# Kernel tuning notes

Measured on AMD Instinct MI355X. Metric: run time of the kernel, lower is better.

## Reference

```python
import jax, jax.numpy as jnp
from jax import lax
import numpy as np
jax.config.update("jax_enable_x64", True)

NUM_CLASSES = 4
RADIUS = 3
POOL = 2
HALF_D = RADIUS ** 3  # 27
_CLIP_MIN = 1e-06
_POS_ALPHA = 0.0005


def setup_inputs() -> dict:
    key = jax.random.key(0)
    k1, k2 = jax.random.split(key)
    logits = jax.random.normal(k1, (2, NUM_CLASSES, 96, 96, 96), dtype=jnp.float32)
    labels = jax.random.randint(k2, (2, 96, 96, 96), 0, NUM_CLASSES).astype(jnp.int64)
    return {"logits": logits, "labels": labels}


def _max_pool3d(x):
    # kernel=stride=POOL over the last three dims of [N,C,H,W,Z]
    return lax.reduce_window(x, -jnp.inf, lax.max,
                             (1, 1, POOL, POOL, POOL), (1, 1, POOL, POOL, POOL), 'VALID')


def _get_pair_vectors(x):
    # x: [N,C,H,W,Z] -> [N,C,HALF_D, (H-R+1)*(W-R+1)*(Z-R+1)] of shifted overlapping copies
    n, c, h, w, z = x.shape
    nh, nw, nz = h - (RADIUS - 1), w - (RADIUS - 1), z - (RADIUS - 1)
    shifts = [x[:, :, i:i + nh, j:j + nw, k:k + nz]
              for i in range(RADIUS) for j in range(RADIUS) for k in range(RADIUS)]
    return jnp.stack(shifts, axis=2).reshape(n, c, HALF_D, -1)


def reference(logits, labels):
    mask = (labels < NUM_CLASSES)                     # [N,H,W,Z] bool
    maskf = mask.astype(jnp.float32)
    onehot = jax.nn.one_hot(labels * mask, NUM_CLASSES, dtype=jnp.float32)  # [N,H,W,Z,C]
    onehot = onehot * maskf[..., None]
    onehot = jnp.transpose(onehot, (0, 4, 1, 2, 3))   # [N,C,H,W,Z]
    probs = jax.nn.sigmoid(logits) * maskf[:, None] + _CLIP_MIN

    la = _max_pool3d(onehot)
    pr = _max_pool3d(probs)

    la_v = _get_pair_vectors(la).astype(jnp.float64)  # [N,C,D,M]
    pr_v = _get_pair_vectors(pr).astype(jnp.float64)

    eye = jnp.eye(HALF_D, dtype=jnp.float64)
    la_v = la_v - la_v.mean(axis=3, keepdims=True)
    pr_v = pr_v - pr_v.mean(axis=3, keepdims=True)
    la_cov = jnp.einsum('ncdm,ncem->ncde', la_v, la_v)
    pr_cov = jnp.einsum('ncdm,ncem->ncde', pr_v, pr_v)
    pr_cov_inv = jnp.linalg.inv(pr_cov + eye * _POS_ALPHA)
    la_pr_cov = jnp.einsum('ncdm,ncem->ncde', la_v, pr_v)
    appro_var = la_cov - la_pr_cov @ pr_cov_inv @ jnp.swapaxes(la_pr_cov, -2, -1)

    chol = jnp.linalg.cholesky(appro_var + eye * _POS_ALPHA)
    diag = jnp.diagonal(chol, axis1=-2, axis2=-1)
    rmi_now = 0.5 * 2.0 * jnp.sum(jnp.log(diag + 1e-08), axis=-1)  # [N,C]
    rmi_per_class = rmi_now.reshape(-1, NUM_CLASSES).mean(axis=0).astype(jnp.float32)
    rmi_per_class = rmi_per_class / float(HALF_D)
    return jnp.sum(rmi_per_class)
```

## Files before the change

kernel.cpp:

```cpp
#include <hip/hip_runtime.h>
#include <math.h>

#define NVAL  97336
#define NCH   8
#define NREP  8
#define GSZ   20480

typedef unsigned short u16;
typedef unsigned int u32;
typedef __attribute__((ext_vector_type(8))) short bf16x8;
typedef __attribute__((ext_vector_type(4))) float f32x4;
typedef __attribute__((ext_vector_type(4))) unsigned int u32x4;

#define LINE_B 336
#define COPY_B 112
#define VOL_B  21504
#define GLINE_U16 48

__global__ __launch_bounds__(256) void pool_kernel(
    const float* __restrict__ logits, const int* __restrict__ labels,
    u16* __restrict__ shifted, float* __restrict__ gacc,
    float* __restrict__ out) {
  int t = blockIdx.x * 256 + threadIdx.x;
  if (t == 0) out[0] = 0.0f;
  for (int z = t; z < NREP * GSZ; z += 432 * 256) gacc[z] = 0.0f;
  int Zp = t % 24; int tmp = t / 24;
  int Y = tmp % 48; tmp /= 48;
  int X = tmp % 48; int n = tmp / 48;
  int sb = (2 * X) * 9216 + (2 * Y) * 96 + 4 * Zp;
  const int4* lb4 = (const int4*)(labels + n * 884736 + sb);
  int4 La = lb4[0], Lb = lb4[24], Lc = lb4[2304], Ld = lb4[2328];
  #pragma unroll
  for (int c = 0; c < 4; c++) {
    const float4* lg4 = (const float4*)(logits + (size_t)(n * 4 + c) * 884736 + sb);
    float4 v0 = lg4[0], v1 = lg4[24], v2 = lg4[2304], v3 = lg4[2328];
    float mx0 = fmaxf(fmaxf(fmaxf(v0.x, v0.y), fmaxf(v1.x, v1.y)),
                      fmaxf(fmaxf(v2.x, v2.y), fmaxf(v3.x, v3.y)));
    float mx1 = fmaxf(fmaxf(fmaxf(v0.z, v0.w), fmaxf(v1.z, v1.w)),
                      fmaxf(fmaxf(v2.z, v2.w), fmaxf(v3.z, v3.w)));
    float pr0 = 1.0f / (1.0f + expf(-mx0)) + 1e-6f;
    float pr1 = 1.0f / (1.0f + expf(-mx1)) + 1e-6f;
    int la0 = (La.x == c || La.y == c || Lb.x == c || Lb.y == c ||
               Lc.x == c || Lc.y == c || Ld.x == c || Ld.y == c);
    int la1 = (La.z == c || La.w == c || Lb.z == c || Lb.w == c ||
               Lc.z == c || Lc.w == c || Ld.z == c || Ld.w == c);
    u32 lapack = (la0 ? 0x3F80u : 0u) | (la1 ? 0x3F800000u : 0u);
    unsigned int q0 = __float_as_uint(pr0);
    unsigned int q1 = __float_as_uint(pr1);
    u32 p0 = (q0 + 0x7FFF + ((q0 >> 16) & 1)) >> 16;
    u32 p1 = (q1 + 0x7FFF + ((q1 >> 16) & 1)) & 0xFFFF0000u;
    u32 prpack = p0 | p1;
    int ch = n * 4 + c;
    int line = X * 48 + Y;
    ((u32*)shifted)[((size_t)(ch * 2 + 0) * 2304 + line) * 24 + Zp] = lapack;
    ((u32*)shifted)[((size_t)(ch * 2 + 1) * 2304 + line) * 24 + Zp] = prpack;
  }
}

#define MFMA16(A, B, C) __builtin_amdgcn_mfma_f32_16x16x32_bf16((A), (B), (C), 0, 0, 0)

#define STEP(BA, AM) do {                                                  \
    int _ba = (BA);                                                        \
    u32x4 ub0 = *(const u32x4*)(smem + _ba + laneC0);                      \
    u32x4 ub1 = *(const u32x4*)(smem + _ba + laneC1);                      \
    u32x4 ub2 = *(const u32x4*)(smem + _ba + laneC2);                      \
    u32x4 ub3 = *(const u32x4*)(smem + _ba + laneC3);                      \
    ub3 = iszero ? zer4 : (isones ? one4 : ub3);                           \
    u32x4 ua0 = ub0, ua1 = ub1, ua2 = ub2, ua3 = ub3;                      \
    ua0.w &= (AM); ua1.w &= (AM); ua2.w &= (AM); ua3.w &= (AM);            \
    bf16x8 A0 = __builtin_bit_cast(bf16x8, ua0);                           \
    bf16x8 A1 = __builtin_bit_cast(bf16x8, ua1);                           \
    bf16x8 A2 = __builtin_bit_cast(bf16x8, ua2);                           \
    bf16x8 A3 = __builtin_bit_cast(bf16x8, ua3);                           \
    bf16x8 B0 = __builtin_bit_cast(bf16x8, ub0);                           \
    bf16x8 B1 = __builtin_bit_cast(bf16x8, ub1);                           \
    bf16x8 B2 = __builtin_bit_cast(bf16x8, ub2);                           \
    bf16x8 B3 = __builtin_bit_cast(bf16x8, ub3);                           \
    acc0 = MFMA16(A0, B0, acc0);  acc1 = MFMA16(A0, B1, acc1);             \
    acc2 = MFMA16(A0, B2, acc2);  acc3 = MFMA16(A0, B3, acc3);             \
    acc4 = MFMA16(A1, B1, acc4);  acc5 = MFMA16(A1, B2, acc5);             \
    acc6 = MFMA16(A1, B3, acc6);  acc7 = MFMA16(A2, B2, acc7);             \
    acc8 = MFMA16(A2, B3, acc8);  acc9 = MFMA16(A3, B3, acc9);             \
  } while (0)

__global__ __launch_bounds__(256) void gram_kernel(
    const u16* __restrict__ shifted, float* __restrict__ gacc) {
  __shared__ __align__(16) unsigned char smem[43008];
  int bx = blockIdx.x;
  int half = bx & 1;
  int tile = (bx >> 1) & 63;
  int ch = bx >> 7;
  int xt = tile >> 3, yt = tile & 7;
  int X0 = xt * 6, Y0 = yt * 6;
  int tw = (xt == 7) ? 4 : 6, th = (yt == 7) ? 4 : 6;
  int tid = threadIdx.x;

  const u16* base = shifted + (size_t)ch * 2 * 2304 * GLINE_U16;
  for (int j = tid; j < 768; j += 256) {
    int chunk = j % 6; int li = j / 6;
    int sy = li & 7, sx = (li >> 3) & 7, vol = li >> 6;
    int gx = X0 + sx; if (gx > 47) gx = 47;
    int gy = Y0 + sy; if (gy > 47) gy = 47;
    const u32* src = (const u32*)(base +
        ((size_t)vol * 2304 + gx * 48 + gy) * GLINE_U16);
    u32x4 v = *(const u32x4*)(src + chunk * 4);
    u32 d4 = (chunk < 5) ? src[chunk * 4 + 4] : 0u;
    unsigned char* dstp = smem + vol * VOL_B + ((sx << 3) + sy) * LINE_B + chunk * 16;
    *(u32x4*)(dstp) = v;
    u32x4 s1 = { (v.x >> 16) | (v.y << 16), (v.y >> 16) | (v.z << 16),
                 (v.z >> 16) | (v.w << 16), (v.w >> 16) | (d4 << 16) };
    *(u32x4*)(dstp + COPY_B) = s1;
    u32x4 s2 = { v.y, v.z, v.w, d4 };
    *(u32x4*)(dstp + 2 * COPY_B) = s2;
  }
  __syncthreads();

  int lane = tid & 63, w = tid >> 6;
  int q = lane >> 4, rlo = lane & 15;
#define LANEC(F) ({ int _r = (F) * 16 + rlo; int _vol = 0, _s = 0;           \
    if (_r < 27) { _s = _r; } else if (_r < 54) { _vol = 1; _s = _r - 27; }  \
    int _dx = _s / 9, _dy = (_s / 3) % 3, _dz = _s % 3;                      \
    _vol * VOL_B + ((_dx << 3) + _dy) * LINE_B + _dz * COPY_B; })
  int laneC0 = LANEC(0), laneC1 = LANEC(1), laneC2 = LANEC(2), laneC3 = LANEC(3);
  unsigned int am1 = (q == 1) ? 0u : ~0u;
  unsigned int am2 = (q == 3) ? 0u : ~0u;
  bool isones = (rlo == 6);
  bool iszero = (rlo > 6);
  u32x4 one4 = {0x3F803F80u, 0x3F803F80u, 0x3F803F80u, 0x3F803F80u};
  u32x4 zer4 = {0u, 0u, 0u, 0u};

  f32x4 acc0 = {0,0,0,0}, acc1 = {0,0,0,0}, acc2 = {0,0,0,0}, acc3 = {0,0,0,0};
  f32x4 acc4 = {0,0,0,0}, acc5 = {0,0,0,0}, acc6 = {0,0,0,0}, acc7 = {0,0,0,0};
  f32x4 acc8 = {0,0,0,0}, acc9 = {0,0,0,0};

  int npl2 = (tw * th) >> 2;
  for (int pl = half * npl2 + w; pl < (half + 1) * npl2; pl += 4) {
    int L0 = 2 * pl, L1 = L0 + 1;
    int lx0 = L0 / th, ly0 = L0 - lx0 * th;
    int lx1 = L1 / th, ly1 = L1 - lx1 * th;
    int U0 = ((lx0 << 3) + ly0) * LINE_B;
    int U1 = ((lx1 << 3) + ly1) * LINE_B;
    STEP(U0 + 16 * q, ~0u);
    STEP((q < 2) ? (U0 + 64 + 16 * q) : (U1 + 16 * q - 32), am1);
    STEP(U1 + 32 + 16 * q, am2);
  }
  __syncthreads();

  float* Pf = (float*)smem;
#define FL(T, A) { float* _qp = Pf + w * 2560 + (T) * 256 + lane;            \
    _qp[0] = (A).x; _qp[64] = (A).y; _qp[128] = (A).z; _qp[192] = (A).w; }
  FL(0, acc0) FL(1, acc1) FL(2, acc2) FL(3, acc3) FL(4, acc4)
  FL(5, acc5) FL(6, acc6) FL(7, acc7) FL(8, acc8) FL(9, acc9)
  __syncthreads();
  float* dst = gacc + (bx & 7) * GSZ + ch * 2560;
  for (int u2 = tid; u2 < 2560; u2 += 256)
    atomicAdd(&dst[u2], Pf[u2] + Pf[u2 + 2560] + Pf[u2 + 5120] + Pf[u2 + 7680]);
}

#define MS 56
__device__ inline double g54(const float* __restrict__ G, int R, int C) {
  int I = R >> 4, J = C >> 4;
  if (I > J) { int tt = R; R = C; C = tt; I = R >> 4; J = C >> 4; }
  int tile = 4 * I - ((I * (I - 1)) >> 1) + (J - I);
  int r = R & 15, c = C & 15;
  return (double)G[tile * 256 + (r & 3) * 64 + ((r >> 2) << 4) + c];
}

__device__ inline int tri_row(int u) {
  int a = (int)((sqrtf(8.0f * (float)u + 1.0f) - 1.0f) * 0.5f);
  while ((a + 1) * (a + 2) / 2 <= u) a++;
  while (a * (a + 1) / 2 > u) a--;
  return a;
}

__global__ __launch_bounds__(256) void stage2_kernel(
    const float* __restrict__ gacc, float* __restrict__ out) {
  __shared__ double M[54 * MS];
  __shared__ float gsf[2560];
  __shared__ double slv[27], spv[27], piv[54], lred[27];
  int ch = blockIdx.x, tid = threadIdx.x;
  const double Minv = 1.0 / (double)NVAL;
  const double alpha = 5e-4;

  for (int u = tid; u < 2560; u += 256) {
    const float* p = gacc + ch * 2560 + u;
    float s = 0.0f;
    #pragma unroll
    for (int r = 0; r < NREP; r++) s += p[r * GSZ];
    gsf[u] = s;
  }
  __syncthreads();
  const float* G = gsf;

  if (tid < 27) { slv[tid] = g54(G, tid, 54); spv[tid] = g54(G, 27 + tid, 54); }
  __syncthreads();
  for (int u = tid; u < 1485; u += 256) {
    int a = tri_row(u);
    int b = u - a * (a + 1) / 2;
    double v;
    if (a < 27) {
      v = g54(G, 27 + a, 27 + b) - spv[a] * spv[b] * Minv + ((a == b) ? alpha : 0.0);
    } else if (b >= 27) {
      int d = a - 27, e = b - 27;
      v = g54(G, d, e) - slv[d] * slv[e] * Minv + ((d == e) ? alpha : 0.0);
    } else {
      v = g54(G, a - 27, 27 + b) - slv[a - 27] * spv[b] * Minv;
    }
    M[a * MS + b] = v;
  }
  __syncthreads();

  #pragma unroll 1
  for (int phase = 0; phase < 6; phase++) {
    int k0 = phase * 8;
    double P[8][8];
    #pragma unroll
    for (int k = 0; k < 8; k++)
      #pragma unroll
      for (int j = 0; j <= k; j++)
        P[k][j] = M[(k0 + k) * MS + (k0 + j)];
    double idv[8];
    #pragma unroll
    for (int k = 0; k < 8; k++) {
      idv[k] = 1.0 / P[k][k];
      #pragma unroll
      for (int i = k + 1; i < 8; i++) {
        double l = P[i][k] * idv[k];
        #pragma unroll
        for (int j = k + 1; j <= i; j++)
          P[i][j] -= l * P[j][k];
      }
      #pragma unroll
      for (int i = k + 1; i < 8; i++) P[i][k] *= idv[k];
    }
    if (tid == 0) {
      #pragma unroll
      for (int k = 0; k < 8; k++) piv[k0 + k] = P[k][k];
    }
    int bstart = k0 + 8, n = 54 - bstart;
    int ncell = n * (n + 1) / 2;
    for (int u = tid; u < ncell; u += 256) {
      int ii = tri_row(u);
      int jj = u - ii * (ii + 1) / 2;
      int i = bstart + ii, j = bstart + jj;
      const double2* Ai = (const double2*)(M + i * MS + k0);
      const double2* Bj = (const double2*)(M + j * MS + k0);
      double2 a01 = Ai[0], a23 = Ai[1], a45 = Ai[2], a67 = Ai[3];
      double2 b01 = Bj[0], b23 = Bj[1], b45 = Bj[2], b67 = Bj[3];
      double av[8] = {a01.x, a01.y, a23.x, a23.y, a45.x, a45.y, a67.x, a67.y};
      double bv[8] = {b01.x, b01.y, b23.x, b23.y, b45.x, b45.y, b67.x, b67.y};
      #pragma unroll
      for (int k = 1; k < 8; k++) {
        #pragma unroll
        for (int m = 0; m < k; m++) {
          av[k] -= P[k][m] * av[m];
          bv[k] -= P[k][m] * bv[m];
        }
      }
      double acc = 0.0;
      #pragma unroll
      for (int k = 0; k < 8; k++) acc += av[k] * (bv[k] * idv[k]);
      M[i * MS + j] -= acc;
    }
    __syncthreads();
  }

  if (tid == 0) {
    double T[6][6];
    #pragma unroll
    for (int k = 0; k < 6; k++)
      #pragma unroll
      for (int j = 0; j <= k; j++)
        T[k][j] = M[(48 + k) * MS + (48 + j)];
    #pragma unroll
    for (int k = 0; k < 6; k++) {
      double dk = T[k][k];
      piv[48 + k] = dk;
      double id = 1.0 / dk;
      #pragma unroll
      for (int i = k + 1; i < 6; i++) {
        double l = T[i][k] * id;
        #pragma unroll
        for (int j = k + 1; j <= i; j++)
          T[i][j] -= l * T[j][k];
      }
    }
  }
  __syncthreads();

  if (tid < 27) lred[tid] = log(sqrt(piv[27 + tid]) + 1e-8);
  __syncthreads();
  if (tid == 0) {
    double s = 0.0;
    for (int i = 0; i < 27; i++) s += lred[i];
    atomicAdd(out, (float)(s / 54.0));
  }
}

extern "C" void kernel_launch(void* const* d_in, const int* in_sizes, int n_in,
                              void* d_out, int out_size, void* d_ws, size_t ws_size,
                              hipStream_t stream) {
  const float* logits = (const float*)d_in[0];
  const int* labels = (const int*)d_in[1];
  float* out = (float*)d_out;

  float* gacc = (float*)d_ws;
  u16* shifted = (u16*)((char*)d_ws + 655360);

  pool_kernel<<<432, 256, 0, stream>>>(logits, labels, shifted, gacc, out);
  gram_kernel<<<1024, 256, 0, stream>>>(shifted, gacc);
  stage2_kernel<<<NCH, 256, 0, stream>>>(gacc, out);
}
```

Measured before the change: 110.1 us.

## Retile gram kernel into 4x4 spatial tiles with smaller LDS and fewer replicas

The gram kernel moves from 8x8-line tiles split into two halves per block to 6x6 halo tiles (4x4 output lines) with one block per tile, giving 1152 blocks and smaller shared memory. The goal is higher occupancy and no duplicated halo loads between the two half-blocks. The number of atomic accumulation replicas drops from 8 to 4, and the four-wave reduction now folds two waves into the other two in LDS first. The trade-off is a larger halo-to-interior ratio, since each block loads 36 lines to compute 16, plus more atomic contention per replica.

```diff
diff --git a/kernel.cpp b/kernel.cpp
--- a/kernel.cpp
+++ b/kernel.cpp
@@ -3,7 +3,7 @@
 
 #define NVAL  97336
 #define NCH   8
-#define NREP  8
+#define NREP  4
 #define GSZ   20480
 
 typedef unsigned short u16;
@@ -14,7 +14,7 @@
 
 #define LINE_B 336
 #define COPY_B 112
-#define VOL_B  21504
+#define VOL_B  12096
 #define GLINE_U16 48
 
 __global__ __launch_bounds__(256) void pool_kernel(
@@ -23,7 +23,7 @@
     float* __restrict__ out) {
   int t = blockIdx.x * 256 + threadIdx.x;
   if (t == 0) out[0] = 0.0f;
-  for (int z = t; z < NREP * GSZ; z += 432 * 256) gacc[z] = 0.0f;
+  if (t < NREP * GSZ) gacc[t] = 0.0f;
   int Zp = t % 24; int tmp = t / 24;
   int Y = tmp % 48; tmp /= 48;
   int X = tmp % 48; int n = tmp / 48;
@@ -85,27 +85,25 @@
 
 __global__ __launch_bounds__(256) void gram_kernel(
     const u16* __restrict__ shifted, float* __restrict__ gacc) {
-  __shared__ __align__(16) unsigned char smem[43008];
+  __shared__ __align__(16) unsigned char smem[24192];
   int bx = blockIdx.x;
-  int half = bx & 1;
-  int tile = (bx >> 1) & 63;
-  int ch = bx >> 7;
-  int xt = tile >> 3, yt = tile & 7;
-  int X0 = xt * 6, Y0 = yt * 6;
-  int tw = (xt == 7) ? 4 : 6, th = (yt == 7) ? 4 : 6;
+  int ch = bx / 144, tile = bx - ch * 144;
+  int xt = tile / 12, yt = tile - xt * 12;
+  int X0 = xt * 4, Y0 = yt * 4;
+  int tw = (xt == 11) ? 2 : 4, th = (yt == 11) ? 2 : 4;
   int tid = threadIdx.x;
 
   const u16* base = shifted + (size_t)ch * 2 * 2304 * GLINE_U16;
-  for (int j = tid; j < 768; j += 256) {
+  for (int j = tid; j < 432; j += 256) {
     int chunk = j % 6; int li = j / 6;
-    int sy = li & 7, sx = (li >> 3) & 7, vol = li >> 6;
+    int sy = li % 6; int t2 = li / 6; int sx = t2 % 6; int vol = t2 / 6;
     int gx = X0 + sx; if (gx > 47) gx = 47;
     int gy = Y0 + sy; if (gy > 47) gy = 47;
     const u32* src = (const u32*)(base +
         ((size_t)vol * 2304 + gx * 48 + gy) * GLINE_U16);
     u32x4 v = *(const u32x4*)(src + chunk * 4);
     u32 d4 = (chunk < 5) ? src[chunk * 4 + 4] : 0u;
-    unsigned char* dstp = smem + vol * VOL_B + ((sx << 3) + sy) * LINE_B + chunk * 16;
+    unsigned char* dstp = smem + vol * VOL_B + (sx * 6 + sy) * LINE_B + chunk * 16;
     *(u32x4*)(dstp) = v;
     u32x4 s1 = { (v.x >> 16) | (v.y << 16), (v.y >> 16) | (v.z << 16),
                  (v.z >> 16) | (v.w << 16), (v.w >> 16) | (d4 << 16) };
@@ -120,7 +118,7 @@
 #define LANEC(F) ({ int _r = (F) * 16 + rlo; int _vol = 0, _s = 0;           \
     if (_r < 27) { _s = _r; } else if (_r < 54) { _vol = 1; _s = _r - 27; }  \
     int _dx = _s / 9, _dy = (_s / 3) % 3, _dz = _s % 3;                      \
-    _vol * VOL_B + ((_dx << 3) + _dy) * LINE_B + _dz * COPY_B; })
+    _vol * VOL_B + (_dx * 6 + _dy) * LINE_B + _dz * COPY_B; })
   int laneC0 = LANEC(0), laneC1 = LANEC(1), laneC2 = LANEC(2), laneC3 = LANEC(3);
   unsigned int am1 = (q == 1) ? 0u : ~0u;
   unsigned int am2 = (q == 3) ? 0u : ~0u;
@@ -133,13 +131,13 @@
   f32x4 acc4 = {0,0,0,0}, acc5 = {0,0,0,0}, acc6 = {0,0,0,0}, acc7 = {0,0,0,0};
   f32x4 acc8 = {0,0,0,0}, acc9 = {0,0,0,0};
 
-  int npl2 = (tw * th) >> 2;
-  for (int pl = half * npl2 + w; pl < (half + 1) * npl2; pl += 4) {
+  int npl = (tw * th) >> 1;
+  for (int pl = w; pl < npl; pl += 4) {
     int L0 = 2 * pl, L1 = L0 + 1;
     int lx0 = L0 / th, ly0 = L0 - lx0 * th;
     int lx1 = L1 / th, ly1 = L1 - lx1 * th;
-    int U0 = ((lx0 << 3) + ly0) * LINE_B;
-    int U1 = ((lx1 << 3) + ly1) * LINE_B;
+    int U0 = (lx0 * 6 + ly0) * LINE_B;
+    int U1 = (lx1 * 6 + ly1) * LINE_B;
     STEP(U0 + 16 * q, ~0u);
     STEP((q < 2) ? (U0 + 64 + 16 * q) : (U1 + 16 * q - 32), am1);
     STEP(U1 + 32 + 16 * q, am2);
@@ -147,14 +145,23 @@
   __syncthreads();
 
   float* Pf = (float*)smem;
-#define FL(T, A) { float* _qp = Pf + w * 2560 + (T) * 256 + lane;            \
+#define FLW(T, A) { float* _qp = Pf + w * 2560 + (T) * 256 + lane;           \
     _qp[0] = (A).x; _qp[64] = (A).y; _qp[128] = (A).z; _qp[192] = (A).w; }
-  FL(0, acc0) FL(1, acc1) FL(2, acc2) FL(3, acc3) FL(4, acc4)
-  FL(5, acc5) FL(6, acc6) FL(7, acc7) FL(8, acc8) FL(9, acc9)
-  __syncthreads();
-  float* dst = gacc + (bx & 7) * GSZ + ch * 2560;
+#define FLA(T, A) { float* _qp = Pf + (w - 2) * 2560 + (T) * 256 + lane;     \
+    _qp[0] += (A).x; _qp[64] += (A).y; _qp[128] += (A).z; _qp[192] += (A).w; }
+  if (w < 2) {
+    FLW(0, acc0) FLW(1, acc1) FLW(2, acc2) FLW(3, acc3) FLW(4, acc4)
+    FLW(5, acc5) FLW(6, acc6) FLW(7, acc7) FLW(8, acc8) FLW(9, acc9)
+  }
+  __syncthreads();
+  if (w >= 2) {
+    FLA(0, acc0) FLA(1, acc1) FLA(2, acc2) FLA(3, acc3) FLA(4, acc4)
+    FLA(5, acc5) FLA(6, acc6) FLA(7, acc7) FLA(8, acc8) FLA(9, acc9)
+  }
+  __syncthreads();
+  float* dst = gacc + (bx & 3) * GSZ + ch * 2560;
   for (int u2 = tid; u2 < 2560; u2 += 256)
-    atomicAdd(&dst[u2], Pf[u2] + Pf[u2 + 2560] + Pf[u2 + 5120] + Pf[u2 + 7680]);
+    atomicAdd(&dst[u2], Pf[u2] + Pf[u2 + 2560]);
 }
 
 #define MS 56
@@ -305,9 +312,9 @@
   float* out = (float*)d_out;
 
   float* gacc = (float*)d_ws;
-  u16* shifted = (u16*)((char*)d_ws + 655360);
+  u16* shifted = (u16*)((char*)d_ws + 327680);
 
   pool_kernel<<<432, 256, 0, stream>>>(logits, labels, shifted, gacc, out);
-  gram_kernel<<<1024, 256, 0, stream>>>(shifted, gacc);
+  gram_kernel<<<NCH * 144, 256, 0, stream>>>(shifted, gacc);
   stage2_kernel<<<NCH, 256, 0, stream>>>(gacc, out);
 }
```

New measurement: 108.8 us. No clear change (-1.2%).
